# Optimization experiments

Measured on AMD Instinct MI355X. Metric: run time of the kernel, lower is better.

## Reference

```python
import jax, jax.numpy as jnp
import numpy as np

D_MODEL = 1024
NUM_HEADS = 16


def setup_inputs() -> dict:
    key = jax.random.key(0)
    ks = jax.random.split(key, 5)
    std = 1.0 / np.sqrt(D_MODEL)
    def w(k):
        return jnp.clip(jax.random.normal(k, (D_MODEL, D_MODEL), dtype=jnp.float32) * std, -3.0, 3.0)
    return {
        "x": jax.random.normal(ks[0], (4, 2048, D_MODEL), dtype=jnp.float32),
        "Wq": w(ks[1]),
        "Wk": w(ks[2]),
        "Wv": w(ks[3]),
        "Wo": w(ks[4]),
    }


def _mha(x, Wq, Wk, Wv, Wo):
    B, S, D = x.shape
    H = NUM_HEADS
    hd = D // H
    # Linear: y = x @ W.T (weights stored [d_out, d_in])
    def proj(W):
        y = jnp.einsum('bsd,ed->bse', x, W)
        return y.reshape(B, S, H, hd).transpose(0, 2, 1, 3)  # b h s d
    q, k, v = proj(Wq), proj(Wk), proj(Wv)
    scores = jnp.einsum('bhqd,bhkd->bhqk', q, k) / np.sqrt(hd)
    causal = jnp.tril(jnp.ones((S, S), dtype=bool))
    scores = jnp.where(causal, scores, -jnp.inf)
    attn = jax.nn.softmax(scores, axis=-1)
    a = jnp.einsum('bhqk,bhkd->bhqd', attn, v)
    a = a.transpose(0, 2, 1, 3).reshape(B, S, D)
    return jnp.einsum('bsd,ed->bse', a, Wo)


def reference(x, Wq, Wk, Wv, Wo):
    return _mha(x, Wq, Wk, Wv, Wo)
```

## Files before the change

### kernel.cpp

```cpp
#include <hip/hip_runtime.h>
#include <hip/hip_bf16.h>
#include <cstdint>
#include <cstddef>


typedef short bf16x8 __attribute__((ext_vector_type(8)));
typedef float f32x4 __attribute__((ext_vector_type(4)));
typedef unsigned int u32x2 __attribute__((ext_vector_type(2)));

__device__ __forceinline__ short f2bf(float f) {
    union { float f; uint32_t u; } c; c.f = f;
    uint32_t r = c.u + 0x7fffu + ((c.u >> 16) & 1u);
    return (short)(r >> 16);
}

__device__ __forceinline__ unsigned cvt_pk_bf16(float lo, float hi) {
    unsigned r;
    asm("v_cvt_pk_bf16_f32 %0, %1, %2" : "=v"(r) : "v"(lo), "v"(hi));
    return r;
}

#define GLOAD_LDS16(g, l) __builtin_amdgcn_global_load_lds( \
    (const __attribute__((address_space(1))) void*)(g),     \
    (__attribute__((address_space(3))) void*)(l), 16, 0, 0)

#define SWZ_RD(base, r, cb) (*(const bf16x8*)((const char*)(base) + (size_t)(r) * 128 + ((cb) ^ (((r) & 7) << 4))))

__global__ __launch_bounds__(256) void convert_all(const float* __restrict__ x,
                                                   const float* __restrict__ w0,
                                                   const float* __restrict__ w1,
                                                   const float* __restrict__ w2,
                                                   const float* __restrict__ w3,
                                                   short* __restrict__ dst) {
    const size_t NX = (size_t)8192 * 1024;
    const size_t NW = (size_t)1024 * 1024;
    int id = blockIdx.x;
    const float* src;
    short* d;
    int i;
    if (id < 4096) {
        src = x; d = dst; i = id * 256 + threadIdx.x;
    } else {
        int idw = id - 4096;
        int wsel = idw >> 9;
        src = (wsel == 0) ? w0 : (wsel == 1) ? w1 : (wsel == 2) ? w2 : w3;
        d = dst + NX + (size_t)wsel * NW;
        i = (idw & 511) * 256 + threadIdx.x;
    }
    const float4* sp = (const float4*)src + (size_t)i * 2;
    float4 v0 = sp[0], v1 = sp[1];
    bf16x8 o;
    o[0] = f2bf(v0.x); o[1] = f2bf(v0.y); o[2] = f2bf(v0.z); o[3] = f2bf(v0.w);
    o[4] = f2bf(v1.x); o[5] = f2bf(v1.y); o[6] = f2bf(v1.z); o[7] = f2bf(v1.w);
    *((bf16x8*)d + i) = o;
}

template<bool OUT_F32>
__device__ __forceinline__ void gemm_body(const short* __restrict__ A,
                                          const short* __restrict__ Bw,
                                          void* __restrict__ Outp,
                                          float escale, bool vtmode) {
    __shared__ __align__(16) short SBUF[2 * 128 * 64];
    short* As = SBUF;
    short* Bs = SBUF + 128 * 64;
    const int tid = threadIdx.x;
    const int lane = tid & 63, w = tid >> 6;
    const int wr = w >> 1, wc = w & 1;
    const int l15 = lane & 15, l4 = lane >> 4;
    const int lin = blockIdx.y * 8 + blockIdx.x;
    const int eff = (lin & 7) * 64 + (lin >> 3);
    const size_t m0 = (size_t)(eff >> 3) * 128;
    const size_t n0 = (size_t)(eff & 7) * 128;

    int srow[4], scol[4];
    #pragma unroll
    for (int i = 0; i < 4; i++) {
        int c = i * 256 + tid;
        srow[i] = c >> 3;
        scol[i] = ((c & 7) ^ (srow[i] & 7)) * 8;
    }

    f32x4 acc[4][4];
    const f32x4 zf = {0.f, 0.f, 0.f, 0.f};
    #pragma unroll
    for (int i = 0; i < 4; i++)
        #pragma unroll
        for (int j = 0; j < 4; j++) acc[i][j] = zf;

    for (int kt = 0; kt < 16; ++kt) {
        const int k0 = kt * 64;
        #pragma unroll
        for (int i = 0; i < 4; i++) {
            GLOAD_LDS16(A  + (m0 + srow[i]) * 1024 + k0 + scol[i], &As[(i * 256 + (w << 6)) * 8]);
            GLOAD_LDS16(Bw + (n0 + srow[i]) * 1024 + k0 + scol[i], &Bs[(i * 256 + (w << 6)) * 8]);
        }
        __syncthreads();

        bf16x8 af[4][2], bfr[4][2];
        #pragma unroll
        for (int mi = 0; mi < 4; mi++) {
            int r = wr * 64 + mi * 16 + l15;
            af[mi][0] = SWZ_RD(As, r, l4 * 16);
            af[mi][1] = SWZ_RD(As, r, 64 + l4 * 16);
        }
        #pragma unroll
        for (int ni = 0; ni < 4; ni++) {
            int r = wc * 64 + ni * 16 + l15;
            bfr[ni][0] = SWZ_RD(Bs, r, l4 * 16);
            bfr[ni][1] = SWZ_RD(Bs, r, 64 + l4 * 16);
        }
        #pragma unroll
        for (int mi = 0; mi < 4; mi++)
            #pragma unroll
            for (int ni = 0; ni < 4; ni++) {
                acc[mi][ni] = __builtin_amdgcn_mfma_f32_16x16x32_bf16(af[mi][0], bfr[ni][0], acc[mi][ni], 0, 0, 0);
                acc[mi][ni] = __builtin_amdgcn_mfma_f32_16x16x32_bf16(af[mi][1], bfr[ni][1], acc[mi][ni], 0, 0, 0);
            }
        __syncthreads();
    }

    if (vtmode) {
        #pragma unroll
        for (int mi = 0; mi < 4; mi++) {
            #pragma unroll
            for (int ni = 0; ni < 4; ni++) {
                int sl  = wr * 64 + mi * 16 + (l4 << 2);
                int col = wc * 64 + ni * 16 + l15;
                u32x2 pr;
                pr[0] = cvt_pk_bf16(acc[mi][ni][0], acc[mi][ni][1]);
                pr[1] = cvt_pk_bf16(acc[mi][ni][2], acc[mi][ni][3]);
                int byte = col * 256 + ((sl * 2) ^ ((col & 7) << 4));
                *(u32x2*)((char*)SBUF + byte) = pr;
            }
        }
        __syncthreads();
        const size_t bb = m0 >> 11, sl0 = m0 & 2047;
        #pragma unroll
        for (int i = 0; i < 8; i++) {
            int c = i * 256 + tid;
            int col = c >> 4, slot = c & 15;
            int byte = col * 256 + ((slot * 16) ^ ((col & 7) << 4));
            bf16x8 v = *(const bf16x8*)((const char*)SBUF + byte);
            *(bf16x8*)&((short*)Outp)[(bb * 1024 + n0 + col) * 2048 + sl0 + slot * 8] = v;
        }
    } else {
        #pragma unroll
        for (int mi = 0; mi < 4; mi++) {
            #pragma unroll
            for (int ni = 0; ni < 4; ni++) {
                size_t row = m0 + wr * 64 + mi * 16 + (l4 << 2);
                size_t col = n0 + wc * 64 + ni * 16 + l15;
                #pragma unroll
                for (int j = 0; j < 4; j++) {
                    float v = acc[mi][ni][j] * escale;
                    if (OUT_F32) ((float*)Outp)[(row + j) * 1024 + col] = v;
                    else         ((short*)Outp)[(row + j) * 1024 + col] = f2bf(v);
                }
            }
        }
    }
}

__global__ __launch_bounds__(256) void gemm_qkv(const short* __restrict__ xb,
                                                const short* __restrict__ Wq,
                                                const short* __restrict__ Wk,
                                                const short* __restrict__ Wv,
                                                short* __restrict__ Q,
                                                short* __restrict__ K,
                                                short* __restrict__ Vt) {
    const short* Bw = (blockIdx.z == 0) ? Wq : (blockIdx.z == 1) ? Wk : Wv;
    short* Out      = (blockIdx.z == 0) ? Q  : (blockIdx.z == 1) ? K  : Vt;
    float sc = (blockIdx.z == 0) ? 0.18033688011112042f : 1.0f;
    gemm_body<false>(xb, Bw, Out, sc, blockIdx.z == 2);
}

__global__ __launch_bounds__(256) void gemm_out(const short* __restrict__ Aw,
                                                const short* __restrict__ Wo,
                                                float* __restrict__ Out) {
    gemm_body<true>(Aw, Wo, Out, 1.0f, false);
}

__global__ __launch_bounds__(512, 4) void attn_kernel(const short* __restrict__ Q,
                                                      const short* __restrict__ K,
                                                      const short* __restrict__ Vt,
                                                      short* __restrict__ Aout) {
    __shared__ __align__(16) short K_lds[2][64 * 64];
    __shared__ __align__(16) short V_lds[2][64 * 64];
    __shared__ __align__(16) short P_lds[8][32][72];
    const int tid = threadIdx.x;
    const int lane = tid & 63, w = tid >> 6;
    const int l15 = lane & 15, l4 = lane >> 4;
    const int bh = blockIdx.x, b = bh >> 4, h = bh & 15;
    const int y = blockIdx.y;
    const int qblk = (y < 4) ? (7 - y) : (y - 4);
    const int qw0 = qblk * 256 + w * 32;
    const short* Qg = Q + (size_t)b * 2048 * 1024 + h * 64;
    const short* Kg = K + (size_t)b * 2048 * 1024 + h * 64;
    const short* Vg = Vt + (size_t)bh * 64 * 2048;

    const int srow = (lane >> 3);
    const int scol = ((lane & 7) ^ srow) * 8;

    bf16x8 qfr[2][2];
    #pragma unroll
    for (int qf = 0; qf < 2; qf++)
        #pragma unroll
        for (int ks = 0; ks < 2; ks++)
            qfr[qf][ks] = *(const bf16x8*)&Qg[(size_t)(qw0 + qf * 16 + l15) * 1024 + ks * 32 + l4 * 8];

    const f32x4 zf = {0.f, 0.f, 0.f, 0.f};
    f32x4 oacc[4][2];
    float l_s[2] = {0.f, 0.f};
    #pragma unroll
    for (int df = 0; df < 4; df++)
        #pragma unroll
        for (int qf = 0; qf < 2; qf++) oacc[df][qf] = zf;

    const int lim = 4 * qblk + 3;

#define KV_RD(base, r, cb) (*(const bf16x8*)((const char*)(base) + (r) * 128 + ((cb) ^ (((r) & 7) << 4))))

    GLOAD_LDS16(Kg + (size_t)(w * 8 + srow) * 1024 + scol, &K_lds[0][w * 512]);
    GLOAD_LDS16(Vg + (size_t)(w * 8 + srow) * 2048 + scol, &V_lds[0][w * 512]);
    __syncthreads();

    int buf = 0;
    for (int t = 0; t <= lim; ++t) {
        const int kv0 = t * 64;
        if (t < lim) {
            const int nv0 = kv0 + 64;
            GLOAD_LDS16(Kg + (size_t)(nv0 + w * 8 + srow) * 1024 + scol, &K_lds[buf ^ 1][w * 512]);
            GLOAD_LDS16(Vg + (size_t)(w * 8 + srow) * 2048 + nv0 + scol, &V_lds[buf ^ 1][w * 512]);
        }

        const int lim_w = (qw0 + 31) >> 6;
        if (t <= lim_w) {
            const short* Kb = K_lds[buf];
            const short* Vb = V_lds[buf];

            f32x4 sacc[4][2];
            #pragma unroll
            for (int kvf = 0; kvf < 4; kvf++)
                #pragma unroll
                for (int qf = 0; qf < 2; qf++) sacc[kvf][qf] = zf;
            __builtin_amdgcn_s_setprio(1);
            #pragma unroll
            for (int kvf = 0; kvf < 4; kvf++) {
                bf16x8 kf0 = KV_RD(Kb, kvf * 16 + l15, l4 * 16);
                bf16x8 kf1 = KV_RD(Kb, kvf * 16 + l15, 64 + l4 * 16);
                #pragma unroll
                for (int qf = 0; qf < 2; qf++) {
                    sacc[kvf][qf] = __builtin_amdgcn_mfma_f32_16x16x32_bf16(kf0, qfr[qf][0], sacc[kvf][qf], 0, 0, 0);
                    sacc[kvf][qf] = __builtin_amdgcn_mfma_f32_16x16x32_bf16(kf1, qfr[qf][1], sacc[kvf][qf], 0, 0, 0);
                }
            }
            __builtin_amdgcn_s_setprio(0);

            if (t == lim_w) {
                #pragma unroll
                for (int kvf = 0; kvf < 4; kvf++)
                    #pragma unroll
                    for (int qf = 0; qf < 2; qf++)
                        #pragma unroll
                        for (int j = 0; j < 4; j++) {
                            int kvg = kv0 + kvf * 16 + l4 * 4 + j;
                            int qg  = qw0 + qf * 16 + l15;
                            if (kvg > qg) sacc[kvf][qf][j] = -1e30f;
                        }
            }

            #pragma unroll
            for (int qf = 0; qf < 2; qf++) {
                float rk[4];
                #pragma unroll
                for (int kvf = 0; kvf < 4; kvf++) {
                    float p0 = __builtin_amdgcn_exp2f(sacc[kvf][qf][0]);
                    float p1 = __builtin_amdgcn_exp2f(sacc[kvf][qf][1]);
                    float p2 = __builtin_amdgcn_exp2f(sacc[kvf][qf][2]);
                    float p3 = __builtin_amdgcn_exp2f(sacc[kvf][qf][3]);
                    sacc[kvf][qf][0] = p0; sacc[kvf][qf][1] = p1;
                    sacc[kvf][qf][2] = p2; sacc[kvf][qf][3] = p3;
                    rk[kvf] = (p0 + p1) + (p2 + p3);
                }
                l_s[qf] += (rk[0] + rk[1]) + (rk[2] + rk[3]);
                #pragma unroll
                for (int kvf = 0; kvf < 4; kvf++) {
                    u32x2 pr;
                    pr[0] = cvt_pk_bf16(sacc[kvf][qf][0], sacc[kvf][qf][1]);
                    pr[1] = cvt_pk_bf16(sacc[kvf][qf][2], sacc[kvf][qf][3]);
                    *(u32x2*)&P_lds[w][qf * 16 + l15][kvf * 16 + l4 * 4] = pr;
                }
            }
            asm volatile("s_waitcnt lgkmcnt(0)" ::: "memory");
            __builtin_amdgcn_sched_barrier(0);

            bf16x8 pf[2][2];
            #pragma unroll
            for (int qf = 0; qf < 2; qf++)
                #pragma unroll
                for (int ks = 0; ks < 2; ks++)
                    pf[qf][ks] = *(const bf16x8*)&P_lds[w][qf * 16 + l15][ks * 32 + l4 * 8];

            __builtin_amdgcn_s_setprio(1);
            #pragma unroll
            for (int df = 0; df < 4; df++) {
                bf16x8 v0 = KV_RD(Vb, df * 16 + l15, l4 * 16);
                bf16x8 v1 = KV_RD(Vb, df * 16 + l15, 64 + l4 * 16);
                #pragma unroll
                for (int qf = 0; qf < 2; qf++) {
                    oacc[df][qf] = __builtin_amdgcn_mfma_f32_16x16x32_bf16(v0, pf[qf][0], oacc[df][qf], 0, 0, 0);
                    oacc[df][qf] = __builtin_amdgcn_mfma_f32_16x16x32_bf16(v1, pf[qf][1], oacc[df][qf], 0, 0, 0);
                }
            }
            __builtin_amdgcn_s_setprio(0);
        }
        __syncthreads();
        buf ^= 1;
    }

    float rl[2];
    #pragma unroll
    for (int qf = 0; qf < 2; qf++) {
        float l = l_s[qf];
        l += __shfl_xor(l, 16);
        l += __shfl_xor(l, 32);
        rl[qf] = 1.f / l;
    }
    #pragma unroll
    for (int qf = 0; qf < 2; qf++)
        #pragma unroll
        for (int df = 0; df < 4; df++) {
            u32x2 pr;
            pr[0] = cvt_pk_bf16(oacc[df][qf][0] * rl[qf], oacc[df][qf][1] * rl[qf]);
            pr[1] = cvt_pk_bf16(oacc[df][qf][2] * rl[qf], oacc[df][qf][3] * rl[qf]);
            *(u32x2*)&P_lds[w][qf * 16 + l15][df * 16 + l4 * 4] = pr;
        }
    asm volatile("s_waitcnt lgkmcnt(0)" ::: "memory");
    __builtin_amdgcn_sched_barrier(0);
    {
        const int r = lane >> 2, cq = lane & 3;
        #pragma unroll
        for (int qf = 0; qf < 2; qf++) {
            size_t orow = (size_t)(b * 2048 + qw0 + qf * 16 + r) * 1024 + h * 64;
            *(bf16x8*)&Aout[orow + cq * 8]       = *(const bf16x8*)&P_lds[w][qf * 16 + r][cq * 8];
            *(bf16x8*)&Aout[orow + (cq + 4) * 8] = *(const bf16x8*)&P_lds[w][qf * 16 + r][(cq + 4) * 8];
        }
    }
#undef KV_RD
}

extern "C" void kernel_launch(void* const* d_in, const int* in_sizes, int n_in,
                              void* d_out, int out_size, void* d_ws, size_t ws_size,
                              hipStream_t stream) {
    const float* x  = (const float*)d_in[0];
    const float* Wq = (const float*)d_in[1];
    const float* Wk = (const float*)d_in[2];
    const float* Wv = (const float*)d_in[3];
    const float* Wo = (const float*)d_in[4];
    float* out = (float*)d_out;

    const size_t NX = (size_t)8192 * 1024;
    const size_t NW = (size_t)1024 * 1024;
    short* xb  = (short*)d_ws;
    short* Wqb = xb  + NX;
    short* Wkb = Wqb + NW;
    short* Wvb = Wkb + NW;
    short* Wob = Wvb + NW;
    short* Qw  = Wob + NW;
    short* Kw  = Qw + NX;
    short* Vt  = (short*)d_out + NX;
    short* Aw  = xb;

    hipLaunchKernelGGL(convert_all, dim3(6144), dim3(256), 0, stream, x, Wq, Wk, Wv, Wo, xb);
    hipLaunchKernelGGL(gemm_qkv, dim3(8, 64, 3), dim3(256), 0, stream, xb, Wqb, Wkb, Wvb, Qw, Kw, Vt);
    hipLaunchKernelGGL(attn_kernel, dim3(64, 8), dim3(512), 0, stream, Qw, Kw, Vt, Aw);
    hipLaunchKernelGGL(gemm_out, dim3(8, 64), dim3(256), 0, stream, Aw, Wob, out);
}
```

Before: 157.4 us.

## Shrink attention blocks to 4 waves over 128 query rows, doubling grid

The attention kernel now uses 256-thread blocks that each cover 128 query rows instead of 512-thread blocks covering 256 rows. The grid becomes a flat 1024 blocks ordered heavy-first, and each wave loads two 16-byte chunks of K/V per tile into LDS. The aim is finer-grained work for better load balance across the causal triangle and more resident blocks per CU. In exchange, each K/V tile is loaded from global memory by twice as many blocks, so reuse per load drops.

```diff
diff --git a/kernel.cpp b/kernel.cpp
--- a/kernel.cpp
+++ b/kernel.cpp
@@ -180,26 +180,32 @@
     gemm_body<true>(Aw, Wo, Out, 1.0f, false);
 }
 
-__global__ __launch_bounds__(512, 4) void attn_kernel(const short* __restrict__ Q,
+__global__ __launch_bounds__(256, 3) void attn_kernel(const short* __restrict__ Q,
                                                       const short* __restrict__ K,
                                                       const short* __restrict__ Vt,
                                                       short* __restrict__ Aout) {
     __shared__ __align__(16) short K_lds[2][64 * 64];
     __shared__ __align__(16) short V_lds[2][64 * 64];
-    __shared__ __align__(16) short P_lds[8][32][72];
+    __shared__ __align__(16) short P_lds[4][32][72];
     const int tid = threadIdx.x;
     const int lane = tid & 63, w = tid >> 6;
     const int l15 = lane & 15, l4 = lane >> 4;
-    const int bh = blockIdx.x, b = bh >> 4, h = bh & 15;
-    const int y = blockIdx.y;
-    const int qblk = (y < 4) ? (7 - y) : (y - 4);
-    const int qw0 = qblk * 256 + w * 32;
+    const int n = blockIdx.x;
+    const int bh = n & 63, b = bh >> 4, h = bh & 15;
+    const int yv = n >> 6;
+    const int qblk = (yv < 8) ? (15 - yv) : (yv - 8);
+    const int qw0 = qblk * 128 + w * 32;
     const short* Qg = Q + (size_t)b * 2048 * 1024 + h * 64;
     const short* Kg = K + (size_t)b * 2048 * 1024 + h * 64;
     const short* Vg = Vt + (size_t)bh * 64 * 2048;
 
-    const int srow = (lane >> 3);
-    const int scol = ((lane & 7) ^ srow) * 8;
+    int sr[2], sc[2];
+    #pragma unroll
+    for (int i = 0; i < 2; i++) {
+        int c = i * 64 + lane;
+        sr[i] = w * 16 + (c >> 3);
+        sc[i] = ((c & 7) ^ (sr[i] & 7)) * 8;
+    }
 
     bf16x8 qfr[2][2];
     #pragma unroll
@@ -216,12 +222,16 @@
         #pragma unroll
         for (int qf = 0; qf < 2; qf++) oacc[df][qf] = zf;
 
-    const int lim = 4 * qblk + 3;
+    const int lim = 2 * qblk + 1;
+    const int lim_w = (qw0 + 31) >> 6;
 
 #define KV_RD(base, r, cb) (*(const bf16x8*)((const char*)(base) + (r) * 128 + ((cb) ^ (((r) & 7) << 4))))
 
-    GLOAD_LDS16(Kg + (size_t)(w * 8 + srow) * 1024 + scol, &K_lds[0][w * 512]);
-    GLOAD_LDS16(Vg + (size_t)(w * 8 + srow) * 2048 + scol, &V_lds[0][w * 512]);
+    #pragma unroll
+    for (int i = 0; i < 2; i++) {
+        GLOAD_LDS16(Kg + (size_t)sr[i] * 1024 + sc[i], &K_lds[0][(w * 128 + i * 64) * 8]);
+        GLOAD_LDS16(Vg + (size_t)sr[i] * 2048 + sc[i], &V_lds[0][(w * 128 + i * 64) * 8]);
+    }
     __syncthreads();
 
     int buf = 0;
@@ -229,11 +239,13 @@
         const int kv0 = t * 64;
         if (t < lim) {
             const int nv0 = kv0 + 64;
-            GLOAD_LDS16(Kg + (size_t)(nv0 + w * 8 + srow) * 1024 + scol, &K_lds[buf ^ 1][w * 512]);
-            GLOAD_LDS16(Vg + (size_t)(w * 8 + srow) * 2048 + nv0 + scol, &V_lds[buf ^ 1][w * 512]);
-        }
-
-        const int lim_w = (qw0 + 31) >> 6;
+            #pragma unroll
+            for (int i = 0; i < 2; i++) {
+                GLOAD_LDS16(Kg + (size_t)(nv0 + sr[i]) * 1024 + sc[i], &K_lds[buf ^ 1][(w * 128 + i * 64) * 8]);
+                GLOAD_LDS16(Vg + (size_t)sr[i] * 2048 + nv0 + sc[i], &V_lds[buf ^ 1][(w * 128 + i * 64) * 8]);
+            }
+        }
+
         if (t <= lim_w) {
             const short* Kb = K_lds[buf];
             const short* Vb = V_lds[buf];
@@ -373,6 +385,6 @@
 
     hipLaunchKernelGGL(convert_all, dim3(6144), dim3(256), 0, stream, x, Wq, Wk, Wv, Wo, xb);
     hipLaunchKernelGGL(gemm_qkv, dim3(8, 64, 3), dim3(256), 0, stream, xb, Wqb, Wkb, Wvb, Qw, Kw, Vt);
-    hipLaunchKernelGGL(attn_kernel, dim3(64, 8), dim3(512), 0, stream, Qw, Kw, Vt, Aw);
+    hipLaunchKernelGGL(attn_kernel, dim3(1024), dim3(256), 0, stream, Qw, Kw, Vt, Aw);
     hipLaunchKernelGGL(gemm_out, dim3(8, 64), dim3(256), 0, stream, Aw, Wob, out);
 }
```

Result: faster. 153.6 us (-2.4%).
